# Kernel optimization log

Measured on AMD Instinct MI355X. Metric: run time of the kernel, lower is better.

The kernel has to match this reference:

```python
import jax, jax.numpy as jnp
import numpy as np

ALPHA = 1.0

def setup_inputs() -> dict:
    key = jax.random.key(0)
    k1, k2 = jax.random.split(key)
    x = jax.random.normal(k1, (65536, 512), dtype=jnp.float32)
    clusters = jax.random.normal(k2, (1024, 512), dtype=jnp.float32)
    return {"x": x, "clusters": clusters}

def reference(x, clusters):
    # same math as sum((x[:,None,:]-c)^2, -1) without the [N,K,D] intermediate)
    x_sq = jnp.sum(x * x, axis=1, keepdims=True)          # [N,1]
    c_sq = jnp.sum(clusters * clusters, axis=1)           # [K]
    cross = x @ clusters.T                                # [N,K]
    dist2 = jnp.maximum(x_sq + c_sq[None, :] - 2.0 * cross, 0.0)
    q = 1.0 / (1.0 + dist2 / ALPHA)
    q = q ** ((ALPHA + 1.0) / 2.0)
    q = q / jnp.sum(q, axis=1, keepdims=True)             # row-normalize
    return q
```

## Files before the change

kernel.cpp:

```cpp
#include <hip/hip_runtime.h>
#include <stdint.h>
#include <stddef.h>

#define DDIM   512
#define KCL    1024
#define BK     32
#define KSTEPS (DDIM / BK)
#define RPB    64
#define THR    1024
#define NROWS  65536
#define NBLK   (NROWS / RPB)

#define SB_BYTES   (KCL * BK * 2)
#define SA_STRIDE  40
#define SA_BYTES   (RPB * SA_STRIDE * 2)
#define SMEM_BYTES (2 * SB_BYTES + 2 * SA_BYTES + 512)

typedef __attribute__((ext_vector_type(4))) float    floatx4;
typedef __attribute__((ext_vector_type(2))) float    floatx2;
typedef __attribute__((ext_vector_type(8))) _Float16 half8;
typedef __attribute__((ext_vector_type(2))) _Float16 half2v;

__device__ __forceinline__ void gload_lds16(const void* g, void* l) {
    __builtin_amdgcn_global_load_lds(
        (const __attribute__((address_space(1))) unsigned char*)g,
        (__attribute__((address_space(3))) unsigned char*)l,
        16, 0, 0);
}

__global__ __launch_bounds__(256) void prep_kernel(const float* __restrict__ clusters,
                                                   _Float16* __restrict__ wsB,
                                                   float* __restrict__ csq) {
    const int l  = threadIdx.x & 63;
    const int c  = (blockIdx.x << 2) + (threadIdx.x >> 6);
    const int ks = l >> 2;
    const int j  = l & 3;

    const float* src = clusters + (size_t)c * DDIM + ks * BK + j * 8;
    floatx4 f0 = *(const floatx4*)src;
    floatx4 f1 = *(const floatx4*)(src + 4);

    half8 h;
    h[0] = (_Float16)f0[0]; h[1] = (_Float16)f0[1]; h[2] = (_Float16)f0[2]; h[3] = (_Float16)f0[3];
    h[4] = (_Float16)f1[0]; h[5] = (_Float16)f1[1]; h[6] = (_Float16)f1[2]; h[7] = (_Float16)f1[3];

    const int p = (j + (c >> 1)) & 3;
    *(half8*)(wsB + (size_t)ks * (KCL * BK) + c * BK + p * 8) = h;

    float ss = f0[0]*f0[0] + f0[1]*f0[1] + f0[2]*f0[2] + f0[3]*f0[3]
             + f1[0]*f1[0] + f1[1]*f1[1] + f1[2]*f1[2] + f1[3]*f1[3];
    ss += __shfl_xor(ss, 1,  64);
    ss += __shfl_xor(ss, 2,  64);
    ss += __shfl_xor(ss, 4,  64);
    ss += __shfl_xor(ss, 8,  64);
    ss += __shfl_xor(ss, 16, 64);
    ss += __shfl_xor(ss, 32, 64);
    if (l == 0) csq[c] = ss;
}

__global__ __launch_bounds__(THR, 4)
void cluster_kernel(const float* __restrict__ x,
                    const _Float16* __restrict__ wsB,
                    const float* __restrict__ csq,
                    float* __restrict__ out) {
    extern __shared__ char smem[];
    char* const sB0 = smem;
    char* const sB1 = smem + SB_BYTES;
    char* const sA0 = smem + 2 * SB_BYTES;
    char* const sA1 = smem + 2 * SB_BYTES + SA_BYTES;
    float* const xsq    = (float*)(smem + 2 * SB_BYTES + 2 * SA_BYTES);
    float* const rowsum = (float*)(smem + 2 * SB_BYTES + 2 * SA_BYTES + 256);

    const int t      = threadIdx.x;
    const int l      = t & 63;
    const int w      = t >> 6;
    const int lane16 = l & 15;
    const int kgrp   = l >> 4;
    const int row0   = blockIdx.x * RPB;
    const int wcol   = w << 6;

    if (t < 64) { xsq[t] = 0.f; rowsum[t] = 0.f; }
    __syncthreads();

    const int abase = lane16 * (SA_STRIDE * 2) + kgrp * 16;
    const int c0    = wcol + lane16;
    const int p0    = (kgrp + (c0 >> 1)) & 3;
    const int bbase = c0 * 64 + p0 * 16;

    const int ar = t >> 4;
    const int ac = (t & 15) << 1;
    const float* const aptr = x + (size_t)(row0 + ar) * DDIM + ac;
    const int awoff = ar * (SA_STRIDE * 2) + ac * 2;

    floatx4 acc[4][4];
#pragma unroll
    for (int rt = 0; rt < 4; ++rt)
#pragma unroll
        for (int ct = 0; ct < 4; ++ct)
            acc[rt][ct] = (floatx4){0.f, 0.f, 0.f, 0.f};

    {
        floatx2 f = __builtin_nontemporal_load((const floatx2*)aptr);
#pragma unroll
        for (int it = 0; it < 4; ++it) {
            const int ch = it * THR + t;
            gload_lds16(wsB + ch * 8, sB0 + ch * 16);
        }
        half2v h;
        h[0] = (_Float16)f[0]; h[1] = (_Float16)f[1];
        *(half2v*)(sA0 + awoff) = h;
        float ss = f[0]*f[0] + f[1]*f[1];
        ss += __shfl_xor(ss, 1, 64);
        ss += __shfl_xor(ss, 2, 64);
        ss += __shfl_xor(ss, 4, 64);
        ss += __shfl_xor(ss, 8, 64);
        if ((t & 15) == 0) atomicAdd(&xsq[ar], ss);
    }

#pragma unroll 2
    for (int k = 0; k < KSTEPS; ++k) {
        char* const sBb = (k & 1) ? sB1 : sB0;
        char* const sAb = (k & 1) ? sA1 : sA0;
        char* const sBn = (k & 1) ? sB0 : sB1;
        char* const sAn = (k & 1) ? sA0 : sA1;

        __syncthreads();

        floatx2 f;
        const bool more = (k + 1 < KSTEPS);
        if (more) {
            f = __builtin_nontemporal_load((const floatx2*)(aptr + (k + 1) * BK));
            const _Float16* wb = wsB + (size_t)(k + 1) * (KCL * BK);
#pragma unroll
            for (int it = 0; it < 4; ++it) {
                const int ch = it * THR + t;
                gload_lds16(wb + ch * 8, sBn + ch * 16);
            }
        }

        half8 aF[4];
#pragma unroll
        for (int rt = 0; rt < 4; ++rt)
            aF[rt] = *(const half8*)(sAb + abase + rt * (16 * SA_STRIDE * 2));
#pragma unroll
        for (int ct = 0; ct < 4; ++ct) {
            const half8 bF = *(const half8*)(sBb + bbase + ct * 1024);
#pragma unroll
            for (int rt = 0; rt < 4; ++rt)
                acc[rt][ct] = __builtin_amdgcn_mfma_f32_16x16x32_f16(aF[rt], bF, acc[rt][ct], 0, 0, 0);
        }

        if (more) {
            half2v h;
            h[0] = (_Float16)f[0]; h[1] = (_Float16)f[1];
            *(half2v*)(sAn + awoff) = h;
            float ss = f[0]*f[0] + f[1]*f[1];
            ss += __shfl_xor(ss, 1, 64);
            ss += __shfl_xor(ss, 2, 64);
            ss += __shfl_xor(ss, 4, 64);
            ss += __shfl_xor(ss, 8, 64);
            if ((t & 15) == 0) atomicAdd(&xsq[ar], ss);
        }
    }

    float cs[4];
#pragma unroll
    for (int ct = 0; ct < 4; ++ct)
        cs[ct] = csq[wcol + ct * 16 + lane16];
    floatx4 xv[4];
#pragma unroll
    for (int rt = 0; rt < 4; ++rt)
        xv[rt] = *(const floatx4*)(xsq + rt * 16 + kgrp * 4);

    float rp[4][4];
#pragma unroll
    for (int rt = 0; rt < 4; ++rt) {
#pragma unroll
        for (int i = 0; i < 4; ++i) {
            const float xr = xv[rt][i];
            float s = 0.f;
#pragma unroll
            for (int ct = 0; ct < 4; ++ct) {
                float d = xr + cs[ct] - 2.0f * acc[rt][ct][i];
                d = fmaxf(d, 0.0f);
                const float q = __builtin_amdgcn_rcpf(1.0f + d);
                acc[rt][ct][i] = q;
                s += q;
            }
            rp[rt][i] = s;
        }
    }
#pragma unroll
    for (int m = 1; m <= 8; m <<= 1)
#pragma unroll
        for (int rt = 0; rt < 4; ++rt)
#pragma unroll
            for (int i = 0; i < 4; ++i)
                rp[rt][i] += __shfl_xor(rp[rt][i], m, 64);
    if (lane16 == 0) {
#pragma unroll
        for (int rt = 0; rt < 4; ++rt)
#pragma unroll
            for (int i = 0; i < 4; ++i)
                atomicAdd(&rowsum[rt * 16 + kgrp * 4 + i], rp[rt][i]);
    }
    __syncthreads();

#pragma unroll
    for (int rt = 0; rt < 4; ++rt) {
        const floatx4 rs = *(const floatx4*)(rowsum + rt * 16 + kgrp * 4);
#pragma unroll
        for (int i = 0; i < 4; ++i) {
            const float inv = __builtin_amdgcn_rcpf(rs[i]);
            float* orow = out + (size_t)(row0 + rt * 16 + kgrp * 4 + i) * KCL + wcol + lane16;
#pragma unroll
            for (int ct = 0; ct < 4; ++ct)
                orow[ct * 16] = acc[rt][ct][i] * inv;
        }
    }
}

extern "C" void kernel_launch(void* const* d_in, const int* in_sizes, int n_in,
                              void* d_out, int out_size, void* d_ws, size_t ws_size,
                              hipStream_t stream) {
    (void)in_sizes; (void)n_in; (void)out_size; (void)ws_size;
    const float* x        = (const float*)d_in[0];
    const float* clusters = (const float*)d_in[1];
    float* out = (float*)d_out;

    _Float16* wsB = (_Float16*)d_ws;
    float*    csq = (float*)((char*)d_ws + (size_t)KSTEPS * KCL * BK * 2);

    hipFuncSetAttribute((const void*)cluster_kernel,
                        hipFuncAttributeMaxDynamicSharedMemorySize, SMEM_BYTES);

    prep_kernel<<<KCL / 4, 256, 0, stream>>>(clusters, wsB, csq);
    cluster_kernel<<<NBLK, THR, SMEM_BYTES, stream>>>(x, wsB, csq, out);
}
```

Measured before the change: 443.4 us.

## Stage full x tile in LDS once, stream B fragments directly from global

Measured after the change: 455.7 us. 1.03x slower.

```diff
diff --git a/kernel.cpp b/kernel.cpp
--- a/kernel.cpp
+++ b/kernel.cpp
@@ -11,22 +11,14 @@
 #define NROWS  65536
 #define NBLK   (NROWS / RPB)
 
-#define SB_BYTES   (KCL * BK * 2)
-#define SA_STRIDE  40
-#define SA_BYTES   (RPB * SA_STRIDE * 2)
-#define SMEM_BYTES (2 * SB_BYTES + 2 * SA_BYTES + 512)
+#define SA_STRIDE_H 520
+#define SA_ROW_B    (SA_STRIDE_H * 2)
+#define SA_BYTES    (RPB * SA_ROW_B)
+#define SMEM_BYTES  (SA_BYTES + 512)
 
 typedef __attribute__((ext_vector_type(4))) float    floatx4;
-typedef __attribute__((ext_vector_type(2))) float    floatx2;
 typedef __attribute__((ext_vector_type(8))) _Float16 half8;
-typedef __attribute__((ext_vector_type(2))) _Float16 half2v;
-
-__device__ __forceinline__ void gload_lds16(const void* g, void* l) {
-    __builtin_amdgcn_global_load_lds(
-        (const __attribute__((address_space(1))) unsigned char*)g,
-        (__attribute__((address_space(3))) unsigned char*)l,
-        16, 0, 0);
-}
+typedef __attribute__((ext_vector_type(4))) _Float16 half4v;
 
 __global__ __launch_bounds__(256) void prep_kernel(const float* __restrict__ clusters,
                                                    _Float16* __restrict__ wsB,
@@ -44,8 +36,7 @@
     h[0] = (_Float16)f0[0]; h[1] = (_Float16)f0[1]; h[2] = (_Float16)f0[2]; h[3] = (_Float16)f0[3];
     h[4] = (_Float16)f1[0]; h[5] = (_Float16)f1[1]; h[6] = (_Float16)f1[2]; h[7] = (_Float16)f1[3];
 
-    const int p = (j + (c >> 1)) & 3;
-    *(half8*)(wsB + (size_t)ks * (KCL * BK) + c * BK + p * 8) = h;
+    *(half8*)(wsB + (size_t)ks * (KCL * BK) + c * BK + j * 8) = h;
 
     float ss = f0[0]*f0[0] + f0[1]*f0[1] + f0[2]*f0[2] + f0[3]*f0[3]
              + f1[0]*f1[0] + f1[1]*f1[1] + f1[2]*f1[2] + f1[3]*f1[3];
@@ -64,12 +55,9 @@
                     const float* __restrict__ csq,
                     float* __restrict__ out) {
     extern __shared__ char smem[];
-    char* const sB0 = smem;
-    char* const sB1 = smem + SB_BYTES;
-    char* const sA0 = smem + 2 * SB_BYTES;
-    char* const sA1 = smem + 2 * SB_BYTES + SA_BYTES;
-    float* const xsq    = (float*)(smem + 2 * SB_BYTES + 2 * SA_BYTES);
-    float* const rowsum = (float*)(smem + 2 * SB_BYTES + 2 * SA_BYTES + 256);
+    char*  const sA     = smem;
+    float* const xsq    = (float*)(smem + SA_BYTES);
+    float* const rowsum = (float*)(smem + SA_BYTES + 256);
 
     const int t      = threadIdx.x;
     const int l      = t & 63;
@@ -82,15 +70,32 @@
     if (t < 64) { xsq[t] = 0.f; rowsum[t] = 0.f; }
     __syncthreads();
 
-    const int abase = lane16 * (SA_STRIDE * 2) + kgrp * 16;
-    const int c0    = wcol + lane16;
-    const int p0    = (kgrp + (c0 >> 1)) & 3;
-    const int bbase = c0 * 64 + p0 * 16;
-
-    const int ar = t >> 4;
-    const int ac = (t & 15) << 1;
-    const float* const aptr = x + (size_t)(row0 + ar) * DDIM + ac;
-    const int awoff = ar * (SA_STRIDE * 2) + ac * 2;
+    {
+#pragma unroll
+        for (int it = 0; it < 8; ++it) {
+            const int g   = it * THR + t;
+            const int row = g >> 7;
+            const int c4  = g & 127;
+            floatx4 f = __builtin_nontemporal_load(
+                (const floatx4*)(x + (size_t)(row0 + row) * DDIM + c4 * 4));
+            half4v h;
+            h[0] = (_Float16)f[0]; h[1] = (_Float16)f[1];
+            h[2] = (_Float16)f[2]; h[3] = (_Float16)f[3];
+            *(half4v*)(sA + row * SA_ROW_B + c4 * 8) = h;
+            float ss = f[0]*f[0] + f[1]*f[1] + f[2]*f[2] + f[3]*f[3];
+            ss += __shfl_xor(ss, 1,  64);
+            ss += __shfl_xor(ss, 2,  64);
+            ss += __shfl_xor(ss, 4,  64);
+            ss += __shfl_xor(ss, 8,  64);
+            ss += __shfl_xor(ss, 16, 64);
+            ss += __shfl_xor(ss, 32, 64);
+            if (l == 0) atomicAdd(&xsq[row], ss);
+        }
+    }
+    __syncthreads();
+
+    const int abase = lane16 * SA_ROW_B + kgrp * 16;
+    const _Float16* const bbase = wsB + (size_t)(wcol + lane16) * BK + kgrp * 8;
 
     floatx4 acc[4][4];
 #pragma unroll
@@ -99,69 +104,39 @@
         for (int ct = 0; ct < 4; ++ct)
             acc[rt][ct] = (floatx4){0.f, 0.f, 0.f, 0.f};
 
-    {
-        floatx2 f = __builtin_nontemporal_load((const floatx2*)aptr);
-#pragma unroll
-        for (int it = 0; it < 4; ++it) {
-            const int ch = it * THR + t;
-            gload_lds16(wsB + ch * 8, sB0 + ch * 16);
-        }
-        half2v h;
-        h[0] = (_Float16)f[0]; h[1] = (_Float16)f[1];
-        *(half2v*)(sA0 + awoff) = h;
-        float ss = f[0]*f[0] + f[1]*f[1];
-        ss += __shfl_xor(ss, 1, 64);
-        ss += __shfl_xor(ss, 2, 64);
-        ss += __shfl_xor(ss, 4, 64);
-        ss += __shfl_xor(ss, 8, 64);
-        if ((t & 15) == 0) atomicAdd(&xsq[ar], ss);
-    }
-
-#pragma unroll 2
-    for (int k = 0; k < KSTEPS; ++k) {
-        char* const sBb = (k & 1) ? sB1 : sB0;
-        char* const sAb = (k & 1) ? sA1 : sA0;
-        char* const sBn = (k & 1) ? sB0 : sB1;
-        char* const sAn = (k & 1) ? sA0 : sA1;
-
-        __syncthreads();
-
-        floatx2 f;
-        const bool more = (k + 1 < KSTEPS);
-        if (more) {
-            f = __builtin_nontemporal_load((const floatx2*)(aptr + (k + 1) * BK));
-            const _Float16* wb = wsB + (size_t)(k + 1) * (KCL * BK);
-#pragma unroll
-            for (int it = 0; it < 4; ++it) {
-                const int ch = it * THR + t;
-                gload_lds16(wb + ch * 8, sBn + ch * 16);
-            }
-        }
-
-        half8 aF[4];
-#pragma unroll
-        for (int rt = 0; rt < 4; ++rt)
-            aF[rt] = *(const half8*)(sAb + abase + rt * (16 * SA_STRIDE * 2));
-#pragma unroll
-        for (int ct = 0; ct < 4; ++ct) {
-            const half8 bF = *(const half8*)(sBb + bbase + ct * 1024);
-#pragma unroll
-            for (int rt = 0; rt < 4; ++rt)
-                acc[rt][ct] = __builtin_amdgcn_mfma_f32_16x16x32_f16(aF[rt], bF, acc[rt][ct], 0, 0, 0);
-        }
-
-        if (more) {
-            half2v h;
-            h[0] = (_Float16)f[0]; h[1] = (_Float16)f[1];
-            *(half2v*)(sAn + awoff) = h;
-            float ss = f[0]*f[0] + f[1]*f[1];
-            ss += __shfl_xor(ss, 1, 64);
-            ss += __shfl_xor(ss, 2, 64);
-            ss += __shfl_xor(ss, 4, 64);
-            ss += __shfl_xor(ss, 8, 64);
-            if ((t & 15) == 0) atomicAdd(&xsq[ar], ss);
-        }
-    }
+    half8 bA[4], bB[4];
+#pragma unroll
+    for (int ct = 0; ct < 4; ++ct)
+        bA[ct] = *(const half8*)(bbase + ct * 512);
+
+#define LOADB(dst, ks_)                                                        \
+    _Pragma("unroll")                                                          \
+    for (int ct = 0; ct < 4; ++ct)                                             \
+        dst[ct] = *(const half8*)(bbase + (size_t)(ks_) * (KCL * BK) + ct * 512);
+
+#define COMPUTE(k_, bsrc)                                                      \
+    {                                                                          \
+        half8 aF[4];                                                           \
+        _Pragma("unroll")                                                      \
+        for (int rt = 0; rt < 4; ++rt)                                         \
+            aF[rt] = *(const half8*)(sA + abase + (k_) * 64 + rt * (16 * SA_ROW_B)); \
+        _Pragma("unroll")                                                      \
+        for (int ct = 0; ct < 4; ++ct)                                         \
+            _Pragma("unroll")                                                  \
+            for (int rt = 0; rt < 4; ++rt)                                     \
+                acc[rt][ct] = __builtin_amdgcn_mfma_f32_16x16x32_f16(          \
+                    aF[rt], bsrc[ct], acc[rt][ct], 0, 0, 0);                   \
+    }
+
+#pragma unroll
+    for (int kk = 0; kk < KSTEPS; kk += 2) {
+        if (kk + 1 < KSTEPS) LOADB(bB, kk + 1);
+        COMPUTE(kk, bA);
+        if (kk + 2 < KSTEPS) LOADB(bA, kk + 2);
+        if (kk + 1 < KSTEPS) COMPUTE(kk + 1, bB);
+    }
+#undef LOADB
+#undef COMPUTE
 
     float cs[4];
 #pragma unroll
```

## Stream B tiles through a 4-slot half-tile LDS ring with replicated workspace copies

Applied to the files above, without the earlier changes.

Result: slower. 479.9 us (+8.2%).

```diff
diff --git a/kernel.cpp b/kernel.cpp
--- a/kernel.cpp
+++ b/kernel.cpp
@@ -11,10 +11,16 @@
 #define NROWS  65536
 #define NBLK   (NROWS / RPB)
 
-#define SB_BYTES   (KCL * BK * 2)
+#define HT_HALVES  16384
+#define HT_BYTES   32768
+#define RING_BYTES (4 * HT_BYTES)
+#define NHALF      32
+#define WSB_HALVES (NHALF * HT_HALVES)
+
 #define SA_STRIDE  40
-#define SA_BYTES   (RPB * SA_STRIDE * 2)
-#define SMEM_BYTES (2 * SB_BYTES + 2 * SA_BYTES + 512)
+#define SA_ROW_B   (SA_STRIDE * 2)
+#define SA_BYTES   (RPB * SA_ROW_B)
+#define SMEM_BYTES (RING_BYTES + 2 * SA_BYTES + 512)
 
 typedef __attribute__((ext_vector_type(4))) float    floatx4;
 typedef __attribute__((ext_vector_type(2))) float    floatx2;
@@ -31,8 +37,10 @@
 __global__ __launch_bounds__(256) void prep_kernel(const float* __restrict__ clusters,
                                                    _Float16* __restrict__ wsB,
                                                    float* __restrict__ csq) {
+    const int blk  = blockIdx.x & 255;
+    const int copy = blockIdx.x >> 8;
     const int l  = threadIdx.x & 63;
-    const int c  = (blockIdx.x << 2) + (threadIdx.x >> 6);
+    const int c  = (blk << 2) + (threadIdx.x >> 6);
     const int ks = l >> 2;
     const int j  = l & 3;
 
@@ -44,32 +52,37 @@
     h[0] = (_Float16)f0[0]; h[1] = (_Float16)f0[1]; h[2] = (_Float16)f0[2]; h[3] = (_Float16)f0[3];
     h[4] = (_Float16)f1[0]; h[5] = (_Float16)f1[1]; h[6] = (_Float16)f1[2]; h[7] = (_Float16)f1[3];
 
-    const int p = (j + (c >> 1)) & 3;
-    *(half8*)(wsB + (size_t)ks * (KCL * BK) + c * BK + p * 8) = h;
-
-    float ss = f0[0]*f0[0] + f0[1]*f0[1] + f0[2]*f0[2] + f0[3]*f0[3]
-             + f1[0]*f1[0] + f1[1]*f1[1] + f1[2]*f1[2] + f1[3]*f1[3];
-    ss += __shfl_xor(ss, 1,  64);
-    ss += __shfl_xor(ss, 2,  64);
-    ss += __shfl_xor(ss, 4,  64);
-    ss += __shfl_xor(ss, 8,  64);
-    ss += __shfl_xor(ss, 16, 64);
-    ss += __shfl_xor(ss, 32, 64);
-    if (l == 0) csq[c] = ss;
+    const int hp   = ks * 2 + (c >> 9);
+    const int cloc = c & 511;
+    const int p    = (j + (cloc >> 1)) & 3;
+    *(half8*)(wsB + (size_t)copy * WSB_HALVES
+                  + (size_t)hp * HT_HALVES + cloc * BK + p * 8) = h;
+
+    if (copy == 0) {
+        float ss = f0[0]*f0[0] + f0[1]*f0[1] + f0[2]*f0[2] + f0[3]*f0[3]
+                 + f1[0]*f1[0] + f1[1]*f1[1] + f1[2]*f1[2] + f1[3]*f1[3];
+        ss += __shfl_xor(ss, 1,  64);
+        ss += __shfl_xor(ss, 2,  64);
+        ss += __shfl_xor(ss, 4,  64);
+        ss += __shfl_xor(ss, 8,  64);
+        ss += __shfl_xor(ss, 16, 64);
+        ss += __shfl_xor(ss, 32, 64);
+        if (l == 0) csq[c] = ss;
+    }
 }
 
 __global__ __launch_bounds__(THR, 4)
 void cluster_kernel(const float* __restrict__ x,
-                    const _Float16* __restrict__ wsB,
+                    const _Float16* __restrict__ wsBall,
                     const float* __restrict__ csq,
-                    float* __restrict__ out) {
+                    float* __restrict__ out,
+                    int ncopy) {
     extern __shared__ char smem[];
-    char* const sB0 = smem;
-    char* const sB1 = smem + SB_BYTES;
-    char* const sA0 = smem + 2 * SB_BYTES;
-    char* const sA1 = smem + 2 * SB_BYTES + SA_BYTES;
-    float* const xsq    = (float*)(smem + 2 * SB_BYTES + 2 * SA_BYTES);
-    float* const rowsum = (float*)(smem + 2 * SB_BYTES + 2 * SA_BYTES + 256);
+    char*  const ring   = smem;
+    char*  const sA0    = smem + RING_BYTES;
+    char*  const sA1    = sA0 + SA_BYTES;
+    float* const xsq    = (float*)(smem + RING_BYTES + 2 * SA_BYTES);
+    float* const rowsum = (float*)(smem + RING_BYTES + 2 * SA_BYTES + 256);
 
     const int t      = threadIdx.x;
     const int l      = t & 63;
@@ -77,20 +90,41 @@
     const int lane16 = l & 15;
     const int kgrp   = l >> 4;
     const int row0   = blockIdx.x * RPB;
-    const int wcol   = w << 6;
+
+    const _Float16* const wb =
+        wsBall + (size_t)(blockIdx.x % ncopy) * WSB_HALVES;
 
     if (t < 64) { xsq[t] = 0.f; rowsum[t] = 0.f; }
     __syncthreads();
 
-    const int abase = lane16 * (SA_STRIDE * 2) + kgrp * 16;
-    const int c0    = wcol + lane16;
-    const int p0    = (kgrp + (c0 >> 1)) & 3;
-    const int bbase = c0 * 64 + p0 * 16;
+    const int abase = lane16 * SA_ROW_B + kgrp * 16;
+    const int cloc0 = (w << 5) + lane16;
+    const int cloc1 = cloc0 + 16;
+    const int boff0 = cloc0 * 64 + ((kgrp + (cloc0 >> 1)) & 3) * 16;
+    const int boff1 = cloc1 * 64 + ((kgrp + (cloc1 >> 1)) & 3) * 16;
 
     const int ar = t >> 4;
     const int ac = (t & 15) << 1;
     const float* const aptr = x + (size_t)(row0 + ar) * DDIM + ac;
-    const int awoff = ar * (SA_STRIDE * 2) + ac * 2;
+    const int awoff = ar * SA_ROW_B + ac * 2;
+
+#define DMAH(hp_) {                                                            \
+        const _Float16* s_ = wb + (size_t)(hp_) * HT_HALVES;                   \
+        char* d_ = ring + ((hp_) & 3) * HT_BYTES;                              \
+        gload_lds16(s_ + t * 8, d_ + t * 16);                                  \
+        gload_lds16(s_ + (1024 + t) * 8, d_ + (1024 + t) * 16);                \
+    }
+
+#define STAGE_A(f_, buf_) {                                                    \
+        half2v h_; h_[0] = (_Float16)(f_)[0]; h_[1] = (_Float16)(f_)[1];       \
+        *(half2v*)((buf_) + awoff) = h_;                                       \
+        float ss_ = (f_)[0]*(f_)[0] + (f_)[1]*(f_)[1];                         \
+        ss_ += __shfl_xor(ss_, 1, 64);                                         \
+        ss_ += __shfl_xor(ss_, 2, 64);                                         \
+        ss_ += __shfl_xor(ss_, 4, 64);                                         \
+        ss_ += __shfl_xor(ss_, 8, 64);                                         \
+        if ((t & 15) == 0) atomicAdd(&xsq[ar], ss_);                           \
+    }
 
     floatx4 acc[4][4];
 #pragma unroll
@@ -99,74 +133,71 @@
         for (int ct = 0; ct < 4; ++ct)
             acc[rt][ct] = (floatx4){0.f, 0.f, 0.f, 0.f};
 
-    {
-        floatx2 f = __builtin_nontemporal_load((const floatx2*)aptr);
-#pragma unroll
-        for (int it = 0; it < 4; ++it) {
-            const int ch = it * THR + t;
-            gload_lds16(wsB + ch * 8, sB0 + ch * 16);
-        }
-        half2v h;
-        h[0] = (_Float16)f[0]; h[1] = (_Float16)f[1];
-        *(half2v*)(sA0 + awoff) = h;
-        float ss = f[0]*f[0] + f[1]*f[1];
-        ss += __shfl_xor(ss, 1, 64);
-        ss += __shfl_xor(ss, 2, 64);
-        ss += __shfl_xor(ss, 4, 64);
-        ss += __shfl_xor(ss, 8, 64);
-        if ((t & 15) == 0) atomicAdd(&xsq[ar], ss);
-    }
-
-#pragma unroll 2
+    floatx2 fA = __builtin_nontemporal_load((const floatx2*)aptr);
+    DMAH(0); DMAH(1);
+    floatx2 fB = __builtin_nontemporal_load((const floatx2*)(aptr + BK));
+    DMAH(2);
+    STAGE_A(fA, sA0);
+    asm volatile("s_waitcnt vmcnt(5) lgkmcnt(0)" ::: "memory");
+    __builtin_amdgcn_s_barrier();
+
+    half8 aF[4];
+#pragma unroll
     for (int k = 0; k < KSTEPS; ++k) {
-        char* const sBb = (k & 1) ? sB1 : sB0;
         char* const sAb = (k & 1) ? sA1 : sA0;
-        char* const sBn = (k & 1) ? sB0 : sB1;
         char* const sAn = (k & 1) ? sA0 : sA1;
-
-        __syncthreads();
-
-        floatx2 f;
-        const bool more = (k + 1 < KSTEPS);
-        if (more) {
-            f = __builtin_nontemporal_load((const floatx2*)(aptr + (k + 1) * BK));
-            const _Float16* wb = wsB + (size_t)(k + 1) * (KCL * BK);
-#pragma unroll
-            for (int it = 0; it < 4; ++it) {
-                const int ch = it * THR + t;
-                gload_lds16(wb + ch * 8, sBn + ch * 16);
-            }
-        }
-
-        half8 aF[4];
-#pragma unroll
-        for (int rt = 0; rt < 4; ++rt)
-            aF[rt] = *(const half8*)(sAb + abase + rt * (16 * SA_STRIDE * 2));
-#pragma unroll
-        for (int ct = 0; ct < 4; ++ct) {
-            const half8 bF = *(const half8*)(sBb + bbase + ct * 1024);
+        {
+            const char* slot = ring + ((2 * k) & 3) * HT_BYTES;
 #pragma unroll
             for (int rt = 0; rt < 4; ++rt)
-                acc[rt][ct] = __builtin_amdgcn_mfma_f32_16x16x32_f16(aF[rt], bF, acc[rt][ct], 0, 0, 0);
-        }
-
-        if (more) {
-            half2v h;
-            h[0] = (_Float16)f[0]; h[1] = (_Float16)f[1];
-            *(half2v*)(sAn + awoff) = h;
-            float ss = f[0]*f[0] + f[1]*f[1];
-            ss += __shfl_xor(ss, 1, 64);
-            ss += __shfl_xor(ss, 2, 64);
-            ss += __shfl_xor(ss, 4, 64);
-            ss += __shfl_xor(ss, 8, 64);
-            if ((t & 15) == 0) atomicAdd(&xsq[ar], ss);
-        }
-    }
+                aF[rt] = *(const half8*)(sAb + abase + rt * (16 * SA_ROW_B));
+            const half8 b0 = *(const half8*)(slot + boff0);
+            const half8 b1 = *(const half8*)(slot + boff1);
+            if (2 * k + 3 <= NHALF - 1) DMAH(2 * k + 3);
+            if (k + 2 <= KSTEPS - 1) {
+                if ((k & 1) == 0)
+                    fA = __builtin_nontemporal_load((const floatx2*)(aptr + (k + 2) * BK));
+                else
+                    fB = __builtin_nontemporal_load((const floatx2*)(aptr + (k + 2) * BK));
+            }
+            asm volatile("s_waitcnt vmcnt(6) lgkmcnt(0)" ::: "memory");
+            __builtin_amdgcn_s_barrier();
+            __builtin_amdgcn_s_setprio(1);
+#pragma unroll
+            for (int rt = 0; rt < 4; ++rt) {
+                acc[rt][0] = __builtin_amdgcn_mfma_f32_16x16x32_f16(aF[rt], b0, acc[rt][0], 0, 0, 0);
+                acc[rt][1] = __builtin_amdgcn_mfma_f32_16x16x32_f16(aF[rt], b1, acc[rt][1], 0, 0, 0);
+            }
+            __builtin_amdgcn_s_setprio(0);
+        }
+        {
+            const char* slot = ring + ((2 * k + 1) & 3) * HT_BYTES;
+            const half8 b2 = *(const half8*)(slot + boff0);
+            const half8 b3 = *(const half8*)(slot + boff1);
+            if (2 * k + 4 <= NHALF - 1) DMAH(2 * k + 4);
+            if (k + 1 <= KSTEPS - 1) {
+                if ((k & 1) == 0) { STAGE_A(fB, sAn); }
+                else              { STAGE_A(fA, sAn); }
+            }
+            asm volatile("s_waitcnt vmcnt(5) lgkmcnt(0)" ::: "memory");
+            __builtin_amdgcn_s_barrier();
+            __builtin_amdgcn_s_setprio(1);
+#pragma unroll
+            for (int rt = 0; rt < 4; ++rt) {
+                acc[rt][2] = __builtin_amdgcn_mfma_f32_16x16x32_f16(aF[rt], b2, acc[rt][2], 0, 0, 0);
+                acc[rt][3] = __builtin_amdgcn_mfma_f32_16x16x32_f16(aF[rt], b3, acc[rt][3], 0, 0, 0);
+            }
+            __builtin_amdgcn_s_setprio(0);
+        }
+    }
+#undef DMAH
+#undef STAGE_A
+    __syncthreads();
 
     float cs[4];
 #pragma unroll
     for (int ct = 0; ct < 4; ++ct)
-        cs[ct] = csq[wcol + ct * 16 + lane16];
+        cs[ct] = csq[(ct >> 1) * 512 + (w << 5) + (ct & 1) * 16 + lane16];
     floatx4 xv[4];
 #pragma unroll
     for (int rt = 0; rt < 4; ++rt)
@@ -212,10 +243,12 @@
 #pragma unroll
         for (int i = 0; i < 4; ++i) {
             const float inv = __builtin_amdgcn_rcpf(rs[i]);
-            float* orow = out + (size_t)(row0 + rt * 16 + kgrp * 4 + i) * KCL + wcol + lane16;
-#pragma unroll
-            for (int ct = 0; ct < 4; ++ct)
-                orow[ct * 16] = acc[rt][ct][i] * inv;
+            float* orow = out + (size_t)(row0 + rt * 16 + kgrp * 4 + i) * KCL
+                        + (w << 5) + lane16;
+            orow[0]            = acc[rt][0][i] * inv;
+            orow[16]           = acc[rt][1][i] * inv;
+            orow[512]          = acc[rt][2][i] * inv;
+            orow[512 + 16]     = acc[rt][3][i] * inv;
         }
     }
 }
@@ -223,17 +256,21 @@
 extern "C" void kernel_launch(void* const* d_in, const int* in_sizes, int n_in,
                               void* d_out, int out_size, void* d_ws, size_t ws_size,
                               hipStream_t stream) {
-    (void)in_sizes; (void)n_in; (void)out_size; (void)ws_size;
+    (void)in_sizes; (void)n_in; (void)out_size;
     const float* x        = (const float*)d_in[0];
     const float* clusters = (const float*)d_in[1];
     float* out = (float*)d_out;
 
+    int ncopy = (int)((ws_size - 4096) / (WSB_HALVES * 2));
+    if (ncopy < 1) ncopy = 1;
+    if (ncopy > 8) ncopy = 8;
+
     _Float16* wsB = (_Float16*)d_ws;
-    float*    csq = (float*)((char*)d_ws + (size_t)KSTEPS * KCL * BK * 2);
+    float*    csq = (float*)((char*)d_ws + (size_t)ncopy * WSB_HALVES * 2);
 
     hipFuncSetAttribute((const void*)cluster_kernel,
                         hipFuncAttributeMaxDynamicSharedMemorySize, SMEM_BYTES);
 
-    prep_kernel<<<KCL / 4, 256, 0, stream>>>(clusters, wsB, csq);
-    cluster_kernel<<<NBLK, THR, SMEM_BYTES, stream>>>(x, wsB, csq, out);
-}
+    prep_kernel<<<256 * ncopy, 256, 0, stream>>>(clusters, wsB, csq);
+    cluster_kernel<<<NBLK, THR, SMEM_BYTES, stream>>>(x, wsB, csq, out, ncopy);
+}
```
